# Performance work log

Hardware: AMD Instinct MI355X
Metric: run time of the kernel (lower is better)

The kernel has to match this reference:

```python
import jax, jax.numpy as jnp
import numpy as np

IN_CH, D, K = 256, 128, 512

def setup_inputs() -> dict:
    key = jax.random.key(0)
    k1, k2, k3, k4 = jax.random.split(key, 4)
    x = jax.random.normal(k1, (16, IN_CH, 64, 64), dtype=jnp.float32)
    W = jax.random.normal(k2, (D, IN_CH), dtype=jnp.float32) * (1.0 / np.sqrt(IN_CH))
    b = jax.random.normal(k3, (D,), dtype=jnp.float32) * 0.01
    prototypes = jax.random.normal(k4, (K, D), dtype=jnp.float32) * 0.02
    gamma = jnp.asarray(1.0, dtype=jnp.float32)
    return {"x": x, "W": W, "b": b, "prototypes": prototypes, "gamma": gamma}

def reference(x, W, b, prototypes, gamma):
    n, c, h, w = x.shape
    # 1x1 conv projection: [n,c,h,w] -> [n,h,w,d]
    q = jnp.einsum('nchw,dc->nhwd', x, W) + b
    q_flat = q.reshape(n * h * w, -1)                      # [T, d]
    q_norm2 = jnp.sum(q_flat * q_flat, axis=1, keepdims=True)   # [T, 1]
    p_norm2 = jnp.sum(prototypes * prototypes, axis=1)[None, :] # [1, K]
    dist2 = q_norm2 + p_norm2 - 2.0 * (q_flat @ prototypes.T)   # [T, K]
    weights = jax.nn.softmax(-jnp.abs(gamma) * dist2, axis=1)
    return weights.reshape(n, h, w, -1).transpose(0, 3, 1, 2)   # [n, K, h, w]
```

## Files before the change

kernel.cpp:

```cpp
#include <hip/hip_runtime.h>

#define HW 4096
#define NCH 256
#define DIM 128
#define NPROTO 512

typedef __attribute__((ext_vector_type(4))) float f32x4;
typedef __attribute__((ext_vector_type(8))) short s16x8;

__device__ __forceinline__ unsigned short f2bf(float f) {
  union { float f; unsigned u; } v; v.f = f;
  unsigned r = v.u + 0x7fffu + ((v.u >> 16) & 1u);
  return (unsigned short)(r >> 16);
}

__device__ __forceinline__ void gload_lds16(const void* g, void* l) {
  __builtin_amdgcn_global_load_lds(
      (const __attribute__((address_space(1))) void*)g,
      (__attribute__((address_space(3))) void*)l, 16, 0, 0);
}

__global__ __launch_bounds__(256) void prep_kernel(const float* __restrict__ P,
                                                   const float* __restrict__ Wm,
                                                   unsigned short* __restrict__ Pr,
                                                   unsigned short* __restrict__ Wbf,
                                                   float* __restrict__ pn2) {
  const int tid = threadIdx.x;
  const int b = blockIdx.x;
  if (b < 8) {
    const int n  = b * 64 + (tid >> 2);
    const int qt = tid & 3;
    const float* row = P + n * DIM + qt * 32;
    unsigned short* dst = Pr + ((size_t)qt * NPROTO + n) * 32;
    float ssq = 0.f;
#pragma unroll
    for (int u = 0; u < 8; ++u) {
      f32x4 v = *(const f32x4*)(row + 4 * u);
      ssq += v.x * v.x + v.y * v.y + v.z * v.z + v.w * v.w;
      dst[4 * u + 0] = f2bf(v.x);
      dst[4 * u + 1] = f2bf(v.y);
      dst[4 * u + 2] = f2bf(v.z);
      dst[4 * u + 3] = f2bf(v.w);
    }
    ssq += __shfl_xor(ssq, 1);
    ssq += __shfl_xor(ssq, 2);
    if (qt == 0) pn2[n] = ssq;
  } else {
    const int idx = ((b - 8) * 256 + tid) * 16;
#pragma unroll
    for (int u = 0; u < 4; ++u) {
      f32x4 v = *(const f32x4*)(Wm + idx + 4 * u);
      unsigned short* d = Wbf + idx + 4 * u;
      d[0] = f2bf(v.x); d[1] = f2bf(v.y); d[2] = f2bf(v.z); d[3] = f2bf(v.w);
    }
  }
}

__global__ __launch_bounds__(512, 6) void fused_kernel(
    const float* __restrict__ x, const unsigned short* __restrict__ Wbf,
    const float* __restrict__ bias, const unsigned short* __restrict__ Pr,
    const float* __restrict__ pn2, const float* __restrict__ gptr,
    float* __restrict__ out) {
  __shared__ __align__(16) char smem[35072];
  unsigned short* q_s = (unsigned short*)smem;
  char* x_b = smem + 8192;
  char* wsb = smem + 17408;
  float* red  = (float*)(smem + 33792);
  float* rmx  = (float*)(smem + 34816);
  float* rinv = (float*)(smem + 34944);

  const int tid  = threadIdx.x;
  const int p0   = blockIdx.x * 32;
  const int nimg = p0 >> 12;
  const int hw0  = p0 & 4095;
  const int wave = tid >> 6, lane = tid & 63;
  const int l15 = lane & 15, l4 = lane >> 4;
  const int wr = wave >> 2, wc = wave & 3;

  f32x4 acc1[2];
#pragma unroll
  for (int j = 0; j < 2; ++j)
#pragma unroll
    for (int r = 0; r < 4; ++r) acc1[j][r] = 0.f;

  const float* xb = x + (size_t)nimg * NCH * HW + hw0;
  const int f  = tid & 7;
  const int cp = tid >> 3;
  const int wrow = 8 * wave + (lane >> 3);
  const int wu   = lane & 7;

#pragma unroll
  for (int t = 0; t < 2; ++t) {
    const int row = 64 * t + wrow;
    gload_lds16(Wbf + (size_t)row * NCH + ((wu ^ (row & 7)) << 3),
                wsb + t * 8192 + wave * 1024);
  }
  f32x4 cv0 = {0,0,0,0}, cv1 = {0,0,0,0};
  if (tid < 256) {
    cv0 = *(const f32x4*)(xb + (size_t)(2 * cp + 0) * HW + 4 * f);
    cv1 = *(const f32x4*)(xb + (size_t)(2 * cp + 1) * HW + 4 * f);
  }

#pragma unroll
  for (int it = 0; it < 4; ++it) {
    const int buf = it & 1;
    const int c0n = 64 * (it + 1);
    f32x4 nv0 = cv0, nv1 = cv1;
    if (tid < 256) {
#pragma unroll
      for (int s = 0; s < 4; ++s) {
        const int row = 4 * f + s;
        unsigned pk = (unsigned)f2bf(cv0[s]) | ((unsigned)f2bf(cv1[s]) << 16);
        *(unsigned*)(x_b + buf * 4608 + row * 144 +
                     ((4 * cp) ^ (((row >> 2) & 7) << 4))) = pk;
      }
      if (it < 3) {
        nv0 = *(const f32x4*)(xb + (size_t)(c0n + 2 * cp + 0) * HW + 4 * f);
        nv1 = *(const f32x4*)(xb + (size_t)(c0n + 2 * cp + 1) * HW + 4 * f);
        asm volatile("s_waitcnt vmcnt(2) lgkmcnt(0)" ::: "memory");
      } else {
        asm volatile("s_waitcnt vmcnt(0) lgkmcnt(0)" ::: "memory");
      }
    } else {
      asm volatile("s_waitcnt vmcnt(0)" ::: "memory");
    }
    __builtin_amdgcn_s_barrier();
#pragma unroll
    for (int kc = 0; kc < 64; kc += 32) {
      const int ub = (kc >> 3) + l4;
      const int row = 16 * wr + l15;
      s16x8 a = *(const s16x8*)(x_b + buf * 4608 + row * 144 +
                                16 * (ub ^ ((row >> 2) & 7)));
#pragma unroll
      for (int j = 0; j < 2; ++j) {
        s16x8 b = *(const s16x8*)(wsb + (32 * wc + 16 * j + l15) * 128 +
                                  ((ub ^ (l15 & 7)) << 4));
        acc1[j] = __builtin_amdgcn_mfma_f32_16x16x32_bf16(a, b, acc1[j], 0, 0, 0);
      }
    }
    asm volatile("s_waitcnt lgkmcnt(0)" ::: "memory");
    __builtin_amdgcn_s_barrier();
    if (it < 3) {
#pragma unroll
      for (int t = 0; t < 2; ++t) {
        const int row = 64 * t + wrow;
        gload_lds16(Wbf + (size_t)row * NCH + c0n + ((wu ^ (row & 7)) << 3),
                    wsb + t * 8192 + wave * 1024);
      }
    }
    cv0 = nv0; cv1 = nv1;
  }

#pragma unroll
  for (int j = 0; j < 2; ++j) {
    const int d = 32 * wc + 16 * j + l15;
    const float bv = bias[d];
    const int u  = d >> 3;
    const int d7 = d & 7;
    const int pxb = 16 * wr + 4 * l4;
#pragma unroll
    for (int r = 0; r < 4; ++r) {
      const int px = pxb + r;
      q_s[px * 128 + ((u ^ (px & 7)) << 3) + d7] = f2bf(acc1[j][r] + bv);
    }
  }

  f32x4 acc[2][4];
#pragma unroll
  for (int i = 0; i < 2; ++i)
#pragma unroll
    for (int j = 0; j < 4; ++j)
#pragma unroll
      for (int r = 0; r < 4; ++r) acc[i][j][r] = 0.f;

  s16x8 bq[4];
#pragma unroll
  for (int j = 0; j < 4; ++j)
    bq[j] = *(const s16x8*)(Pr + (size_t)(64 * wave + 16 * j + l15) * 32 + 8 * l4);
  __syncthreads();

#pragma unroll
  for (int ch = 0; ch < 4; ++ch) {
    s16x8 afr[2];
#pragma unroll
    for (int i = 0; i < 2; ++i) {
      const int px = 16 * i + l15;
      afr[i] = *(const s16x8*)&q_s[px * 128 + (((4 * ch + l4) ^ (px & 7)) << 3)];
    }
#pragma unroll
    for (int j = 0; j < 4; ++j)
#pragma unroll
      for (int i = 0; i < 2; ++i)
        acc[i][j] = __builtin_amdgcn_mfma_f32_16x16x32_bf16(afr[i], bq[j], acc[i][j], 0, 0, 0);
    if (ch < 3) {
      __builtin_amdgcn_sched_barrier(0);
#pragma unroll
      for (int j = 0; j < 4; ++j)
        bq[j] = *(const s16x8*)(Pr + (size_t)((ch + 1) * NPROTO + 64 * wave + 16 * j + l15) * 32 + 8 * l4);
    }
  }

  const float g2  = fabsf(gptr[0]) * 1.44269504088896340736f;
  const float tg2 = 2.f * g2;
  float cj[4];
#pragma unroll
  for (int j = 0; j < 4; ++j) cj[j] = g2 * pn2[64 * wave + 16 * j + l15];

#pragma unroll
  for (int i = 0; i < 2; ++i)
#pragma unroll
    for (int r = 0; r < 4; ++r) {
      float m = -1e30f;
#pragma unroll
      for (int j = 0; j < 4; ++j) {
        float lv = fmaf(acc[i][j][r], tg2, -cj[j]);
        acc[i][j][r] = lv;
        m = fmaxf(m, lv);
      }
#pragma unroll
      for (int s = 1; s < 16; s <<= 1) m = fmaxf(m, __shfl_xor(m, s));
      if (l15 == 0) red[wave * 32 + 16 * i + 4 * l4 + r] = m;
    }
  __syncthreads();
  if (tid < 32) {
    float M = red[tid];
#pragma unroll
    for (int w = 1; w < 8; ++w) M = fmaxf(M, red[w * 32 + tid]);
    rmx[tid] = M;
  }
  __syncthreads();

#pragma unroll
  for (int i = 0; i < 2; ++i) {
    const f32x4 Mi = *(const f32x4*)&rmx[16 * i + 4 * l4];
#pragma unroll
    for (int r = 0; r < 4; ++r) {
      float s = 0.f;
#pragma unroll
      for (int j = 0; j < 4; ++j) {
        float e = exp2f(acc[i][j][r] - Mi[r]);
        acc[i][j][r] = e;
        s += e;
      }
#pragma unroll
      for (int t = 1; t < 16; t <<= 1) s += __shfl_xor(s, t);
      if (l15 == 0) red[wave * 32 + 16 * i + 4 * l4 + r] = s;
    }
  }
  __syncthreads();
  if (tid < 32) {
    float S = 0.f;
#pragma unroll
    for (int w = 0; w < 8; ++w) S += red[w * 32 + tid];
    rinv[tid] = 1.f / S;
  }
  __syncthreads();

  float* ob = out + (size_t)nimg * NPROTO * HW + hw0;
#pragma unroll
  for (int i = 0; i < 2; ++i) {
    const f32x4 iv = *(const f32x4*)&rinv[16 * i + 4 * l4];
    const int px = 16 * i + 4 * l4;
#pragma unroll
    for (int j = 0; j < 4; ++j) {
      const int k = 64 * wave + 16 * j + l15;
      f32x4 o = acc[i][j] * iv;
      *(f32x4*)(ob + (size_t)k * HW + px) = o;
    }
  }
}

extern "C" void kernel_launch(void* const* d_in, const int* in_sizes, int n_in,
                              void* d_out, int out_size, void* d_ws, size_t ws_size,
                              hipStream_t stream) {
  const float* x     = (const float*)d_in[0];
  const float* Wm    = (const float*)d_in[1];
  const float* bias  = (const float*)d_in[2];
  const float* prot  = (const float*)d_in[3];
  const float* gamma = (const float*)d_in[4];
  float* out = (float*)d_out;

  unsigned short* Pr_w  = (unsigned short*)d_ws;
  float*          pn2_w = (float*)((char*)d_ws + 131072);
  unsigned short* W_ws  = (unsigned short*)((char*)d_ws + 131072 + 2048);

  prep_kernel<<<16, 256, 0, stream>>>(prot, Wm, Pr_w, W_ws, pn2_w);
  fused_kernel<<<2048, 512, 0, stream>>>(x, W_ws, bias, Pr_w, pn2_w, gamma, out);
}
```

Measured before the change: 218.7 us.

## Keep W fragments in registers and prefetch all x loads upfront in fused kernel

The first GEMM (x to q projection) now has each wave own 16 output channels and hold its bf16 W fragments in registers, loaded directly from global memory. This removes the LDS staging buffer for W and the per-iteration async copies. All four x chunks are issued as loads up front, and the prototype fragments for the second GEMM are double-buffered one chunk ahead. LDS use drops, but register pressure rises and the occupancy hint falls from 6 to 4 blocks, which may reduce latency hiding. One barrier per iteration is removed, yet x_b is double-buffered with only one barrier per iteration, which may risk a write-after-read race two iterations apart.

```diff
diff --git a/kernel.cpp b/kernel.cpp
--- a/kernel.cpp
+++ b/kernel.cpp
@@ -12,12 +12,6 @@
   union { float f; unsigned u; } v; v.f = f;
   unsigned r = v.u + 0x7fffu + ((v.u >> 16) & 1u);
   return (unsigned short)(r >> 16);
-}
-
-__device__ __forceinline__ void gload_lds16(const void* g, void* l) {
-  __builtin_amdgcn_global_load_lds(
-      (const __attribute__((address_space(1))) void*)g,
-      (__attribute__((address_space(3))) void*)l, 16, 0, 0);
 }
 
 __global__ __launch_bounds__(256) void prep_kernel(const float* __restrict__ P,
@@ -56,18 +50,17 @@
   }
 }
 
-__global__ __launch_bounds__(512, 6) void fused_kernel(
+__global__ __launch_bounds__(512, 4) void fused_kernel(
     const float* __restrict__ x, const unsigned short* __restrict__ Wbf,
     const float* __restrict__ bias, const unsigned short* __restrict__ Pr,
     const float* __restrict__ pn2, const float* __restrict__ gptr,
     float* __restrict__ out) {
-  __shared__ __align__(16) char smem[35072];
+  __shared__ __align__(16) char smem[18688];
   unsigned short* q_s = (unsigned short*)smem;
   char* x_b = smem + 8192;
-  char* wsb = smem + 17408;
-  float* red  = (float*)(smem + 33792);
-  float* rmx  = (float*)(smem + 34816);
-  float* rinv = (float*)(smem + 34944);
+  float* red  = (float*)(smem + 17408);
+  float* rmx  = (float*)(smem + 18432);
+  float* rinv = (float*)(smem + 18560);
 
   const int tid  = threadIdx.x;
   const int p0   = blockIdx.x * 32;
@@ -75,93 +68,73 @@
   const int hw0  = p0 & 4095;
   const int wave = tid >> 6, lane = tid & 63;
   const int l15 = lane & 15, l4 = lane >> 4;
-  const int wr = wave >> 2, wc = wave & 3;
-
-  f32x4 acc1[2];
-#pragma unroll
-  for (int j = 0; j < 2; ++j)
-#pragma unroll
-    for (int r = 0; r < 4; ++r) acc1[j][r] = 0.f;
+
+  const int dloc = 16 * wave + l15;
+  s16x8 wf[8];
+  {
+    const unsigned short* wrow = Wbf + (size_t)dloc * NCH + 8 * l4;
+#pragma unroll
+    for (int k = 0; k < 8; ++k) wf[k] = *(const s16x8*)(wrow + 32 * k);
+  }
 
   const float* xb = x + (size_t)nimg * NCH * HW + hw0;
   const int f  = tid & 7;
   const int cp = tid >> 3;
-  const int wrow = 8 * wave + (lane >> 3);
-  const int wu   = lane & 7;
-
-#pragma unroll
-  for (int t = 0; t < 2; ++t) {
-    const int row = 64 * t + wrow;
-    gload_lds16(Wbf + (size_t)row * NCH + ((wu ^ (row & 7)) << 3),
-                wsb + t * 8192 + wave * 1024);
-  }
-  f32x4 cv0 = {0,0,0,0}, cv1 = {0,0,0,0};
+  f32x4 xv[4][2];
   if (tid < 256) {
-    cv0 = *(const f32x4*)(xb + (size_t)(2 * cp + 0) * HW + 4 * f);
-    cv1 = *(const f32x4*)(xb + (size_t)(2 * cp + 1) * HW + 4 * f);
-  }
+#pragma unroll
+    for (int it = 0; it < 4; ++it) {
+      xv[it][0] = *(const f32x4*)(xb + (size_t)(64 * it + 2 * cp + 0) * HW + 4 * f);
+      xv[it][1] = *(const f32x4*)(xb + (size_t)(64 * it + 2 * cp + 1) * HW + 4 * f);
+    }
+  }
+  const float bv = bias[dloc];
+
+  f32x4 acc1[2];
+#pragma unroll
+  for (int i = 0; i < 2; ++i)
+#pragma unroll
+    for (int r = 0; r < 4; ++r) acc1[i][r] = 0.f;
 
 #pragma unroll
   for (int it = 0; it < 4; ++it) {
-    const int buf = it & 1;
-    const int c0n = 64 * (it + 1);
-    f32x4 nv0 = cv0, nv1 = cv1;
+    char* xbuf = x_b + (it & 1) * 4608;
     if (tid < 256) {
 #pragma unroll
       for (int s = 0; s < 4; ++s) {
         const int row = 4 * f + s;
-        unsigned pk = (unsigned)f2bf(cv0[s]) | ((unsigned)f2bf(cv1[s]) << 16);
-        *(unsigned*)(x_b + buf * 4608 + row * 144 +
-                     ((4 * cp) ^ (((row >> 2) & 7) << 4))) = pk;
-      }
-      if (it < 3) {
-        nv0 = *(const f32x4*)(xb + (size_t)(c0n + 2 * cp + 0) * HW + 4 * f);
-        nv1 = *(const f32x4*)(xb + (size_t)(c0n + 2 * cp + 1) * HW + 4 * f);
-        asm volatile("s_waitcnt vmcnt(2) lgkmcnt(0)" ::: "memory");
-      } else {
-        asm volatile("s_waitcnt vmcnt(0) lgkmcnt(0)" ::: "memory");
-      }
-    } else {
-      asm volatile("s_waitcnt vmcnt(0)" ::: "memory");
-    }
+        unsigned pk = (unsigned)f2bf(xv[it][0][s]) | ((unsigned)f2bf(xv[it][1][s]) << 16);
+        *(unsigned*)(xbuf + row * 144 + ((4 * cp) ^ (((row >> 2) & 7) << 4))) = pk;
+      }
+    }
+    asm volatile("s_waitcnt lgkmcnt(0)" ::: "memory");
     __builtin_amdgcn_s_barrier();
 #pragma unroll
     for (int kc = 0; kc < 64; kc += 32) {
       const int ub = (kc >> 3) + l4;
-      const int row = 16 * wr + l15;
-      s16x8 a = *(const s16x8*)(x_b + buf * 4608 + row * 144 +
-                                16 * (ub ^ ((row >> 2) & 7)));
-#pragma unroll
-      for (int j = 0; j < 2; ++j) {
-        s16x8 b = *(const s16x8*)(wsb + (32 * wc + 16 * j + l15) * 128 +
-                                  ((ub ^ (l15 & 7)) << 4));
-        acc1[j] = __builtin_amdgcn_mfma_f32_16x16x32_bf16(a, b, acc1[j], 0, 0, 0);
-      }
-    }
-    asm volatile("s_waitcnt lgkmcnt(0)" ::: "memory");
-    __builtin_amdgcn_s_barrier();
-    if (it < 3) {
-#pragma unroll
-      for (int t = 0; t < 2; ++t) {
-        const int row = 64 * t + wrow;
-        gload_lds16(Wbf + (size_t)row * NCH + c0n + ((wu ^ (row & 7)) << 3),
-                    wsb + t * 8192 + wave * 1024);
-      }
-    }
-    cv0 = nv0; cv1 = nv1;
-  }
-
-#pragma unroll
-  for (int j = 0; j < 2; ++j) {
-    const int d = 32 * wc + 16 * j + l15;
-    const float bv = bias[d];
-    const int u  = d >> 3;
-    const int d7 = d & 7;
-    const int pxb = 16 * wr + 4 * l4;
-#pragma unroll
-    for (int r = 0; r < 4; ++r) {
-      const int px = pxb + r;
-      q_s[px * 128 + ((u ^ (px & 7)) << 3) + d7] = f2bf(acc1[j][r] + bv);
+      s16x8 a[2];
+#pragma unroll
+      for (int i = 0; i < 2; ++i) {
+        const int row = 16 * i + l15;
+        a[i] = *(const s16x8*)(xbuf + row * 144 + 16 * (ub ^ ((row >> 2) & 7)));
+      }
+#pragma unroll
+      for (int i = 0; i < 2; ++i)
+        acc1[i] = __builtin_amdgcn_mfma_f32_16x16x32_bf16(a[i], wf[2 * it + (kc >> 5)],
+                                                          acc1[i], 0, 0, 0);
+    }
+  }
+
+  {
+    const int u = dloc >> 3, d7 = dloc & 7;
+#pragma unroll
+    for (int i = 0; i < 2; ++i) {
+      const int pxb = 16 * i + 4 * l4;
+#pragma unroll
+      for (int r = 0; r < 4; ++r) {
+        const int px = pxb + r;
+        q_s[px * 128 + ((u ^ (px & 7)) << 3) + d7] = f2bf(acc1[i][r] + bv);
+      }
     }
   }
 
@@ -173,32 +146,39 @@
 #pragma unroll
       for (int r = 0; r < 4; ++r) acc[i][j][r] = 0.f;
 
-  s16x8 bq[4];
-#pragma unroll
-  for (int j = 0; j < 4; ++j)
-    bq[j] = *(const s16x8*)(Pr + (size_t)(64 * wave + 16 * j + l15) * 32 + 8 * l4);
-  __syncthreads();
-
-#pragma unroll
-  for (int ch = 0; ch < 4; ++ch) {
-    s16x8 afr[2];
-#pragma unroll
-    for (int i = 0; i < 2; ++i) {
-      const int px = 16 * i + l15;
-      afr[i] = *(const s16x8*)&q_s[px * 128 + (((4 * ch + l4) ^ (px & 7)) << 3)];
-    }
-#pragma unroll
-    for (int j = 0; j < 4; ++j)
-#pragma unroll
-      for (int i = 0; i < 2; ++i)
-        acc[i][j] = __builtin_amdgcn_mfma_f32_16x16x32_bf16(afr[i], bq[j], acc[i][j], 0, 0, 0);
-    if (ch < 3) {
-      __builtin_amdgcn_sched_barrier(0);
-#pragma unroll
-      for (int j = 0; j < 4; ++j)
-        bq[j] = *(const s16x8*)(Pr + (size_t)((ch + 1) * NPROTO + 64 * wave + 16 * j + l15) * 32 + 8 * l4);
-    }
-  }
+  s16x8 bqA[4], bqB[4];
+#pragma unroll
+  for (int j = 0; j < 4; ++j)
+    bqA[j] = *(const s16x8*)(Pr + (size_t)(0 * NPROTO + 64 * wave + 16 * j + l15) * 32 + 8 * l4);
+#pragma unroll
+  for (int j = 0; j < 4; ++j)
+    bqB[j] = *(const s16x8*)(Pr + (size_t)(1 * NPROTO + 64 * wave + 16 * j + l15) * 32 + 8 * l4);
+  asm volatile("s_waitcnt lgkmcnt(0)" ::: "memory");
+  __builtin_amdgcn_s_barrier();
+
+#define DO_CHUNK(CH, BQ)                                                        \
+  {                                                                             \
+    s16x8 afr[2];                                                               \
+    _Pragma("unroll") for (int i = 0; i < 2; ++i) {                             \
+      const int px = 16 * i + l15;                                              \
+      afr[i] = *(const s16x8*)&q_s[px * 128 + (((4 * (CH) + l4) ^ (px & 7)) << 3)]; \
+    }                                                                           \
+    _Pragma("unroll") for (int j = 0; j < 4; ++j)                               \
+      _Pragma("unroll") for (int i = 0; i < 2; ++i)                             \
+        acc[i][j] = __builtin_amdgcn_mfma_f32_16x16x32_bf16(afr[i], BQ[j], acc[i][j], 0, 0, 0); \
+  }
+
+  DO_CHUNK(0, bqA);
+#pragma unroll
+  for (int j = 0; j < 4; ++j)
+    bqA[j] = *(const s16x8*)(Pr + (size_t)(2 * NPROTO + 64 * wave + 16 * j + l15) * 32 + 8 * l4);
+  DO_CHUNK(1, bqB);
+#pragma unroll
+  for (int j = 0; j < 4; ++j)
+    bqB[j] = *(const s16x8*)(Pr + (size_t)(3 * NPROTO + 64 * wave + 16 * j + l15) * 32 + 8 * l4);
+  DO_CHUNK(2, bqA);
+  DO_CHUNK(3, bqB);
+#undef DO_CHUNK
 
   const float g2  = fabsf(gptr[0]) * 1.44269504088896340736f;
   const float tg2 = 2.f * g2;
```

Result: no change. 220.2 us (+0.7%).
